# Kernel optimization log

Measured on AMD Instinct MI355X. Metric: run time of the kernel, lower is better.

The kernel has to match this reference:

```python
import jax, jax.numpy as jnp
import numpy as np

NEG_SLOPE = 0.2

def gat_conv(x, src, dst, W, a_s, a_d, b, num_nodes, heads, out_c, concat):
    # x: [N, F_in]; W: [F_in, heads*out_c]; a_s/a_d: [heads, out_c]
    h = (x @ W).reshape(num_nodes, heads, out_c)          # [N,H,C]
    alpha_src = jnp.sum(h * a_s, axis=-1)                 # [N,H]
    alpha_dst = jnp.sum(h * a_d, axis=-1)                 # [N,H]
    e = jax.nn.leaky_relu(alpha_src[src] + alpha_dst[dst], NEG_SLOPE)  # [E,H]
    m = jax.ops.segment_max(e, dst, num_segments=num_nodes)           # [N,H]
    e = jnp.exp(e - m[dst])
    s = jax.ops.segment_sum(e, dst, num_segments=num_nodes)
    alpha = e / (s[dst] + 1e-16)                          # [E,H]
    out = jax.ops.segment_sum(h[src] * alpha[:, :, None], dst, num_segments=num_nodes)  # [N,H,C]
    if concat:
        out = out.reshape(num_nodes, heads * out_c)
    else:
        out = out.mean(axis=1)
    return out + b


def setup_inputs() -> dict:
    key = jax.random.key(0)
    ks = jax.random.split(key, 16)
    N, E, P = 50000, 800000, 200000
    F_in, Hd, C_out, H = 128, 32, 64, 4
    inp = {
        'x': jax.random.normal(ks[0], (N, F_in), dtype=jnp.float32),
        'edge_index': jax.random.randint(ks[1], (2, E), 0, N, dtype=jnp.int32),
        'edge_pairs': jax.random.randint(ks[2], (2, P), 0, N, dtype=jnp.int32),
        'W1': jax.random.normal(ks[3], (F_in, H * Hd), dtype=jnp.float32) * 0.05,
        'att_src1': jax.random.normal(ks[4], (H, Hd), dtype=jnp.float32) * 0.05,
        'att_dst1': jax.random.normal(ks[5], (H, Hd), dtype=jnp.float32) * 0.05,
        'b1': jnp.zeros((H * Hd,), dtype=jnp.float32),
        'W2': jax.random.normal(ks[6], (H * Hd, C_out), dtype=jnp.float32) * 0.05,
        'att_src2': jax.random.normal(ks[7], (1, C_out), dtype=jnp.float32) * 0.05,
        'att_dst2': jax.random.normal(ks[8], (1, C_out), dtype=jnp.float32) * 0.05,
        'b2': jnp.zeros((C_out,), dtype=jnp.float32),
        'Wm1': jax.random.normal(ks[9], (2 * C_out, Hd), dtype=jnp.float32) * 0.05,
        'bm1': jnp.zeros((Hd,), dtype=jnp.float32),
        'Wm2': jax.random.normal(ks[10], (Hd, 1), dtype=jnp.float32) * 0.05,
        'bm2': jnp.zeros((1,), dtype=jnp.float32),
    }
    return inp


def reference(x, edge_index, edge_pairs, W1, att_src1, att_dst1, b1,
              W2, att_src2, att_dst2, b2, Wm1, bm1, Wm2, bm2):
    N = x.shape[0]
    # add self-loops (PyG GATConv default)
    loop = jnp.arange(N, dtype=edge_index.dtype)
    src = jnp.concatenate([edge_index[0], loop])
    dst = jnp.concatenate([edge_index[1], loop])
    h = gat_conv(x, src, dst, W1, att_src1, att_dst1, b1, N, 4, 32, concat=True)
    h = jax.nn.elu(h)
    h = gat_conv(h, src, dst, W2, att_src2, att_dst2, b2, N, 1, 64, concat=True)
    ps, pd = edge_pairs[0], edge_pairs[1]
    ef = jnp.concatenate([h[ps], h[pd]], axis=-1)          # [P, 2*C_out]
    out = jax.nn.relu(ef @ Wm1 + bm1) @ Wm2 + bm2          # [P,1]
    return out[:, 0]
```

## Files before the change

kernel.cpp:

```cpp
#include <hip/hip_runtime.h>
#include <hip/hip_bf16.h>
#include <hip/hip_fp16.h>


#define LRELU_SLOPE 0.2f
#define BKT_SH 7
#define NB_MAX 512

typedef _Float16 v8h __attribute__((ext_vector_type(8)));
typedef float    v4f __attribute__((ext_vector_type(4)));

__global__ void __launch_bounds__(256) zero_prep_kernel(
    const float* __restrict__ W1, const float* __restrict__ W2,
    const float* __restrict__ Wm1,
    _Float16* __restrict__ W1Th, _Float16* __restrict__ W2Th,
    float* __restrict__ Wm1T, uint4* __restrict__ zp, int zn4)
{
    int i = blockIdx.x * 256 + threadIdx.x;
    if (i < zn4) zp[i] = make_uint4(0u, 0u, 0u, 0u);
    if (i < 16384) {
        int k = i >> 7, j = i & 127;
        W1Th[j * 128 + k] = (_Float16)W1[i];
    } else if (i < 16384 + 8192) {
        int t = i - 16384;
        int k = t >> 6, j = t & 63;
        W2Th[j * 128 + k] = (_Float16)W2[t];
    } else if (i < 16384 + 8192 + 4096) {
        int t = i - 24576;
        int k = t >> 5, j = t & 31;
        Wm1T[j * 128 + k] = Wm1[t];
    }
}

template<int AHALF>
__device__ __forceinline__ void gemm_att_body(
    int bx, int by,
    const void* __restrict__ Xv, const _Float16* __restrict__ WTH,
    const float* __restrict__ atts, const float* __restrict__ attd,
    _Float16* __restrict__ OUT, float* __restrict__ oas, float* __restrict__ oad,
    int N, int ncols, int H, int headShift)
{
    __shared__ _Float16 cs[64 * 68];
    int tid = threadIdx.x;
    int lane = tid & 63;
    int wv = tid >> 6;
    int rowBase = bx * 64 + wv * 16;
    int colBase = by * 64;
    int lr = lane & 15;
    int lk = lane >> 4;

    v8h bf[4][4];
    #pragma unroll
    for (int ct = 0; ct < 4; ct++) {
        const _Float16* bp = WTH + (size_t)(colBase + ct * 16 + lr) * 128 + lk * 8;
        #pragma unroll
        for (int ks = 0; ks < 4; ks++)
            bf[ct][ks] = *(const v8h*)(bp + ks * 32);
    }

    int arow = rowBase + lr;
    if (arow >= N) arow = N - 1;
    v4f acc[4];
    #pragma unroll
    for (int ct = 0; ct < 4; ct++) acc[ct] = (v4f){0.f, 0.f, 0.f, 0.f};

    if (AHALF) {
        const _Float16* ap = (const _Float16*)Xv + (size_t)arow * 128 + lk * 8;
        #pragma unroll
        for (int ks = 0; ks < 4; ks++) {
            v8h af = *(const v8h*)(ap + ks * 32);
            #pragma unroll
            for (int ct = 0; ct < 4; ct++)
                acc[ct] = __builtin_amdgcn_mfma_f32_16x16x32_f16(af, bf[ct][ks],
                                                                 acc[ct], 0, 0, 0);
        }
    } else {
        const float* ap = (const float*)Xv + (size_t)arow * 128 + lk * 8;
        #pragma unroll
        for (int ks = 0; ks < 4; ks++) {
            float4 a0 = *(const float4*)(ap + ks * 32);
            float4 a1 = *(const float4*)(ap + ks * 32 + 4);
            v8h af;
            af[0] = (_Float16)a0.x; af[1] = (_Float16)a0.y;
            af[2] = (_Float16)a0.z; af[3] = (_Float16)a0.w;
            af[4] = (_Float16)a1.x; af[5] = (_Float16)a1.y;
            af[6] = (_Float16)a1.z; af[7] = (_Float16)a1.w;
            #pragma unroll
            for (int ct = 0; ct < 4; ct++)
                acc[ct] = __builtin_amdgcn_mfma_f32_16x16x32_f16(af, bf[ct][ks],
                                                                 acc[ct], 0, 0, 0);
        }
    }

    int ctPerHead = (1 << headShift) >> 4;
    #pragma unroll
    for (int hh = 0; hh < 2; hh++) {
        if (hh * ctPerHead >= 4) break;
        float ps[4] = {0.f, 0.f, 0.f, 0.f};
        float pd[4] = {0.f, 0.f, 0.f, 0.f};
        for (int c2 = 0; c2 < ctPerHead; c2++) {
            int ct = hh * ctPerHead + c2;
            int col = colBase + ct * 16 + lr;
            float ws = atts[col], wd = attd[col];
            #pragma unroll
            for (int r = 0; r < 4; r++) {
                ps[r] = fmaf(acc[ct][r], ws, ps[r]);
                pd[r] = fmaf(acc[ct][r], wd, pd[r]);
            }
        }
        #pragma unroll
        for (int r = 0; r < 4; r++) {
            #pragma unroll
            for (int m = 1; m < 16; m <<= 1) {
                ps[r] += __shfl_xor(ps[r], m);
                pd[r] += __shfl_xor(pd[r], m);
            }
        }
        if (lr == 0) {
            int head = (colBase >> headShift) + hh;
            #pragma unroll
            for (int r = 0; r < 4; r++) {
                int row = rowBase + lk * 4 + r;
                if (row < N) {
                    oas[(size_t)row * H + head] = ps[r];
                    oad[(size_t)row * H + head] = pd[r];
                }
            }
        }
    }

    #pragma unroll
    for (int ct = 0; ct < 4; ct++)
        #pragma unroll
        for (int r = 0; r < 4; r++)
            cs[(wv * 16 + lk * 4 + r) * 68 + ct * 16 + lr] = (_Float16)acc[ct][r];
    __syncthreads();
    int rr = tid >> 2;
    int cb = (tid & 3) * 16;
    int grow = bx * 64 + rr;
    if (grow < N) {
        const uint4* sp = (const uint4*)(cs + rr * 68 + cb);
        _Float16* op = OUT + (size_t)grow * ncols + colBase + cb;
        uint4 w0 = sp[0];
        uint4 w1 = sp[1];
        *(uint4*)op = w0;
        *(uint4*)(op + 8) = w1;
    }
}

__global__ void __launch_bounds__(256) gemm1_hist_kernel(
    const float* __restrict__ X, const _Float16* __restrict__ WTH,
    const float* __restrict__ atts, const float* __restrict__ attd,
    _Float16* __restrict__ OUT, float* __restrict__ oas, float* __restrict__ oad,
    int N, int nbG,
    const int* __restrict__ dst, int E, int* __restrict__ deg)
{
    if ((int)blockIdx.x < 2 * nbG) {
        gemm_att_body<0>(blockIdx.x % nbG, blockIdx.x / nbG, X, WTH, atts, attd,
                         OUT, oas, oad, N, 128, 4, 5);
    } else {
        int i = ((int)blockIdx.x - 2 * nbG) * 256 + threadIdx.x;
        if (i < E + N) {
            int d = (i < E) ? dst[i] : (i - E);
            atomicAdd(deg + d, 1);
        }
    }
}

__global__ void __launch_bounds__(256) gemm2_kernel(
    const _Float16* __restrict__ X, const _Float16* __restrict__ WTH,
    const float* __restrict__ atts, const float* __restrict__ attd,
    _Float16* __restrict__ OUT, float* __restrict__ oas, float* __restrict__ oad,
    int N)
{
    gemm_att_body<1>(blockIdx.x, 0, X, WTH, atts, attd, OUT, oas, oad,
                     N, 64, 1, 6);
}

__global__ void __launch_bounds__(1024) scan1_kernel(
    const int* __restrict__ deg, int* __restrict__ rowp,
    int* __restrict__ btot, int n)
{
    __shared__ int wsum[16];
    int t = threadIdx.x, lane = t & 63, wid = t >> 6;
    int idx = blockIdx.x * 1024 + t;
    int v = (idx < n) ? deg[idx] : 0;
    #pragma unroll
    for (int off = 1; off < 64; off <<= 1) {
        int y = __shfl_up(v, off);
        if (lane >= off) v += y;
    }
    if (lane == 63) wsum[wid] = v;
    __syncthreads();
    if (wid == 0) {
        int s = (lane < 16) ? wsum[lane] : 0;
        #pragma unroll
        for (int off = 1; off < 16; off <<= 1) {
            int y = __shfl_up(s, off);
            if (lane >= off) s += y;
        }
        if (lane < 16) wsum[lane] = s;
    }
    __syncthreads();
    if (wid > 0) v += wsum[wid - 1];
    if (idx < n) rowp[idx + 1] = v;
    if (t == 1023) btot[blockIdx.x] = v;
    if (idx == 0) rowp[0] = 0;
}

__global__ void __launch_bounds__(1024) scan23_kernel(
    int* __restrict__ rowp, const int* __restrict__ btot, int n)
{
    int b = blockIdx.x;
    if (b == 0) return;
    __shared__ int soff;
    int t = threadIdx.x;
    if (t < 64) {
        int v = (t < b) ? btot[t] : 0;
        #pragma unroll
        for (int m = 1; m < 64; m <<= 1) v += __shfl_xor(v, m);
        if (t == 0) soff = v;
    }
    __syncthreads();
    int idx = b * 1024 + t;
    if (idx < n) rowp[idx + 1] += soff;
}

__global__ void __launch_bounds__(256) bin_kernel(
    const int* __restrict__ src, const int* __restrict__ dst, int E, int N,
    const int* __restrict__ rowp, int* __restrict__ bcur,
    uint2* __restrict__ ebuf, int nbkt)
{
    __shared__ int lcnt[NB_MAX];
    __shared__ int loff[NB_MAX];
    __shared__ int lbase[NB_MAX];
    int tid = threadIdx.x;
    int EN = E + N;
    int base = blockIdx.x * 4096;
    for (int b = tid; b < nbkt; b += 256) { lcnt[b] = 0; loff[b] = 0; }
    __syncthreads();
    #pragma unroll
    for (int j = 0; j < 16; j++) {
        int i = base + j * 256 + tid;
        if (i < EN) {
            int d = (i < E) ? dst[i] : (i - E);
            atomicAdd(&lcnt[d >> BKT_SH], 1);
        }
    }
    __syncthreads();
    for (int b = tid; b < nbkt; b += 256) {
        int c = lcnt[b];
        lbase[b] = c ? atomicAdd(&bcur[b], c) : 0;
    }
    __syncthreads();
    #pragma unroll
    for (int j = 0; j < 16; j++) {
        int i = base + j * 256 + tid;
        if (i < EN) {
            int s, d;
            if (i < E) { s = src[i]; d = dst[i]; } else { s = d = i - E; }
            int b = d >> BKT_SH;
            int off = atomicAdd(&loff[b], 1);
            int nb0 = b << BKT_SH;
            int start = rowp[nb0 > N ? N : nb0];
            ebuf[(size_t)start + lbase[b] + off] = make_uint2((unsigned)d, (unsigned)s);
        }
    }
}

__global__ void __launch_bounds__(256) scatter2_kernel(
    const uint2* __restrict__ ebuf, const int* __restrict__ rowp,
    int* __restrict__ csrs, int N)
{
    __shared__ int lcur[1 << BKT_SH];
    int b = blockIdx.x;
    int n0 = b << BKT_SH;
    int n1 = n0 + (1 << BKT_SH); if (n1 > N) n1 = N;
    if (n0 >= N) return;
    for (int i = threadIdx.x; i < (1 << BKT_SH); i += 256) lcur[i] = 0;
    __syncthreads();
    int r0 = rowp[n0], r1 = rowp[n1];
    for (int i = r0 + threadIdx.x; i < r1; i += 256) {
        uint2 e = ebuf[i];
        int d = (int)e.x;
        int pos = rowp[d] + atomicAdd(&lcur[d - n0], 1);
        csrs[pos] = (int)e.y;
    }
}

template<int K>
__device__ __forceinline__ void chunk1(
    const int* __restrict__ csr, int base, int cnt,
    const float* __restrict__ as1, float adv,
    int el, int hh, int hd, int lane, const __half2* __restrict__ h1,
    float& accx, float& accy, float& srun)
{
    float wvA = 0.f, wvB = 0.f;
    if (el < cnt) {
        int s = csr[base + el];
        float e = as1[s * 4 + hh] + adv;
        e = e > 0.f ? e : LRELU_SLOPE * e;
        wvA = __expf(e);
    }
    if (K > 16 && el + 16 < cnt) {
        int s = csr[base + 16 + el];
        float e = as1[s * 4 + hh] + adv;
        e = e > 0.f ? e : LRELU_SLOPE * e;
        wvB = __expf(e);
    }
    float t = wvA + wvB;
    t += __shfl_xor(t, 4);  t += __shfl_xor(t, 8);
    t += __shfl_xor(t, 16); t += __shfl_xor(t, 32);
    srun += t;
    __half2 hv[K];
    #pragma unroll
    for (int e2 = 0; e2 < K; ++e2) {
        int ee = e2 < cnt ? e2 : cnt - 1;
        int s = csr[base + ee];
        hv[e2] = h1[(size_t)s * 64 + lane];
    }
    #pragma unroll
    for (int e2 = 0; e2 < K; ++e2) {
        float av = (e2 < 16) ? __shfl(wvA, (e2 << 2) | hd)
                             : __shfl(wvB, ((e2 - 16) << 2) | hd);
        float2 v = __half22float2(hv[e2]);
        accx = fmaf(av, v.x, accx);
        accy = fmaf(av, v.y, accy);
    }
}

__global__ void __launch_bounds__(256) edge1_kernel(
    const int* __restrict__ csr, const int* __restrict__ rowp,
    const __half2* __restrict__ h1, const float* __restrict__ as1,
    const float* __restrict__ ad1, const float* __restrict__ b1,
    __half* __restrict__ x2h, int N)
{
    int lane = threadIdx.x & 63;
    int n = __builtin_amdgcn_readfirstlane(blockIdx.x * 4 + (threadIdx.x >> 6));
    if (n >= N) return;
    int rs = rowp[n], re = rowp[n + 1];
    int hd = lane >> 4;
    int el = lane >> 2, hh = lane & 3;
    float adv = ad1[n * 4 + hh];
    float accx = 0.f, accy = 0.f, srun = 0.f;
    int base = rs, rem = re - rs;
    while (rem >= 32) {
        chunk1<32>(csr, base, 32, as1, adv, el, hh, hd, lane, h1, accx, accy, srun);
        base += 32; rem -= 32;
    }
    if (rem > 24)      chunk1<32>(csr, base, rem, as1, adv, el, hh, hd, lane, h1, accx, accy, srun);
    else if (rem > 16) chunk1<24>(csr, base, rem, as1, adv, el, hh, hd, lane, h1, accx, accy, srun);
    else if (rem > 8)  chunk1<16>(csr, base, rem, as1, adv, el, hh, hd, lane, h1, accx, accy, srun);
    else if (rem > 0)  chunk1<8> (csr, base, rem, as1, adv, el, hh, hd, lane, h1, accx, accy, srun);

    float sden = __shfl(srun, hd) + 1e-16f;
    float inv = 1.f / sden;
    float2 bv = *(const float2*)(b1 + lane * 2);
    float o0 = accx * inv + bv.x;
    float o1 = accy * inv + bv.y;
    o0 = o0 > 0.f ? o0 : (__expf(o0) - 1.f);
    o1 = o1 > 0.f ? o1 : (__expf(o1) - 1.f);
    *(__half2*)(x2h + (size_t)n * 128 + lane * 2) = __floats2half2_rn(o0, o1);
}

template<int K>
__device__ __forceinline__ void chunk2(
    const int* __restrict__ csr, int base, int cnt,
    const float* __restrict__ as2, float adv, int lane,
    const __half* __restrict__ h2, float& acc, float& srun)
{
    float wv = 0.f;
    if (lane < cnt) {
        int s = csr[base + lane];
        float e = as2[s] + adv;
        e = e > 0.f ? e : LRELU_SLOPE * e;
        wv = __expf(e);
    }
    srun += wv;
    __half hv[K];
    #pragma unroll
    for (int e2 = 0; e2 < K; ++e2) {
        int ee = e2 < cnt ? e2 : cnt - 1;
        int s = csr[base + ee];
        hv[e2] = h2[(size_t)s * 64 + lane];
    }
    #pragma unroll
    for (int e2 = 0; e2 < K; ++e2) {
        float av = __shfl(wv, e2);
        acc = fmaf(av, __half2float(hv[e2]), acc);
    }
}

__global__ void __launch_bounds__(256) edge2_kernel(
    const int* __restrict__ csr, const int* __restrict__ rowp,
    const __half* __restrict__ h2, const float* __restrict__ as2,
    const float* __restrict__ ad2, const float* __restrict__ b2,
    float* __restrict__ hf, int N)
{
    int lane = threadIdx.x & 63;
    int n = __builtin_amdgcn_readfirstlane(blockIdx.x * 4 + (threadIdx.x >> 6));
    if (n >= N) return;
    int rs = rowp[n], re = rowp[n + 1];
    float adv = ad2[n];
    float acc = 0.f, srun = 0.f;
    int base = rs, rem = re - rs;
    while (rem >= 16) {
        chunk2<16>(csr, base, 16, as2, adv, lane, h2, acc, srun);
        base += 16; rem -= 16;
    }
    if (rem > 8)      chunk2<16>(csr, base, rem, as2, adv, lane, h2, acc, srun);
    else if (rem > 0) chunk2<8> (csr, base, rem, as2, adv, lane, h2, acc, srun);

    #pragma unroll
    for (int m = 1; m < 64; m <<= 1) srun += __shfl_xor(srun, m);
    float o = acc / (srun + 1e-16f) + b2[lane];
    hf[(size_t)n * 64 + lane] = o;
}

__global__ void __launch_bounds__(256) node_mlp_kernel(
    const float* __restrict__ hf, const float* __restrict__ Wm1T,
    __half* __restrict__ uv, int N)
{
    int lane = threadIdx.x & 63;
    int j = lane & 31, half = lane >> 5;
    const float* wr = Wm1T + j * 128 + half * 64;
    float wreg[64];
    #pragma unroll
    for (int q = 0; q < 16; q++) {
        float4 t = ((const float4*)wr)[q];
        wreg[q*4] = t.x; wreg[q*4+1] = t.y; wreg[q*4+2] = t.z; wreg[q*4+3] = t.w;
    }
    int wgid = __builtin_amdgcn_readfirstlane(blockIdx.x * 4 + (threadIdx.x >> 6));
    int nwaves = gridDim.x * 4;
    for (int n = wgid; n < N; n += nwaves) {
        const float* hr = hf + (size_t)n * 64;
        float acc = 0.f;
        #pragma unroll
        for (int k = 0; k < 64; k += 4) {
            float4 hv = *(const float4*)(hr + k);
            acc = fmaf(hv.x, wreg[k],   acc);
            acc = fmaf(hv.y, wreg[k+1], acc);
            acc = fmaf(hv.z, wreg[k+2], acc);
            acc = fmaf(hv.w, wreg[k+3], acc);
        }
        uv[(size_t)n * 64 + lane] = __float2half_rn(acc);
    }
}

__global__ void __launch_bounds__(256) pair_mlp_kernel(
    const int* __restrict__ ps, const int* __restrict__ pd,
    const __half2* __restrict__ uv, const float* __restrict__ bm1,
    const float* __restrict__ Wm2, const float* __restrict__ bm2,
    float* __restrict__ out, int P)
{
    int gid = blockIdx.x * 256 + threadIdx.x;
    int p = gid >> 1;
    if (p >= P) return;
    int half = gid & 1;
    int j0 = half * 8;
    int a = ps[p], b = pd[p];
    const __half2* ua = uv + (size_t)a * 32 + j0;
    const __half2* vb = uv + (size_t)b * 32 + 16 + j0;
    float r = 0.f;
    #pragma unroll
    for (int q = 0; q < 8; q++) {
        float2 uu = __half22float2(ua[q]);
        float2 vv = __half22float2(vb[q]);
        float2 bb = *(const float2*)(bm1 + half * 16 + q * 2);
        float2 ww = *(const float2*)(Wm2 + half * 16 + q * 2);
        float h0 = uu.x + vv.x + bb.x; h0 = h0 > 0.f ? h0 : 0.f; r = fmaf(h0, ww.x, r);
        float h1 = uu.y + vv.y + bb.y; h1 = h1 > 0.f ? h1 : 0.f; r = fmaf(h1, ww.y, r);
    }
    r += __shfl_xor(r, 1);
    if (half == 0) out[p] = r + bm2[0];
}

extern "C" void kernel_launch(void* const* d_in, const int* in_sizes, int n_in,
                              void* d_out, int out_size, void* d_ws, size_t ws_size,
                              hipStream_t stream)
{
    const float* x    = (const float*)d_in[0];
    const int*   ei   = (const int*)  d_in[1];
    const int*   ep   = (const int*)  d_in[2];
    const float* W1   = (const float*)d_in[3];
    const float* atS1 = (const float*)d_in[4];
    const float* atD1 = (const float*)d_in[5];
    const float* b1   = (const float*)d_in[6];
    const float* W2   = (const float*)d_in[7];
    const float* atS2 = (const float*)d_in[8];
    const float* atD2 = (const float*)d_in[9];
    const float* b2   = (const float*)d_in[10];
    const float* Wm1  = (const float*)d_in[11];
    const float* bm1  = (const float*)d_in[12];
    const float* Wm2  = (const float*)d_in[13];
    const float* bm2  = (const float*)d_in[14];
    float* out = (float*)d_out;

    int N = in_sizes[0] / 128;
    int E = in_sizes[1] / 2;
    int P = in_sizes[2] / 2;
    int Etot = E + N;

    char* w = (char*)d_ws;
    auto alloc = [&](size_t bytes) {
        char* p = w; w += (bytes + 255) & ~(size_t)255; return p;
    };
    _Float16* W1Th = (_Float16*)alloc(16384 * 2);
    _Float16* W2Th = (_Float16*)alloc(8192 * 2);
    float*    Wm1T = (float*)alloc(4096 * 4);
    _Float16* h1   = (_Float16*)alloc((size_t)N * 128 * 2);
    __half*   x2h  = (__half*)alloc((size_t)N * 128 * 2);
    _Float16* h2   = (_Float16*)alloc((size_t)N * 64 * 2);
    float*    hf   = (float*)alloc((size_t)N * 64 * 4);
    int*      rowp = (int*)alloc((size_t)(N + 1) * 4);
    int*      btot = (int*)alloc(64 * 4);
    int*      csrs = (int*)alloc((size_t)Etot * 4);
    uint2*    ebuf = (uint2*)alloc((size_t)Etot * 8);
    char* z0 = w;
    int*   deg  = (int*)alloc((size_t)N * 4);
    int*   bcur = (int*)alloc(NB_MAX * 4);
    char* z1 = w;
    float* as1  = (float*)alloc((size_t)N * 4 * 4);
    float* ad1  = (float*)alloc((size_t)N * 4 * 4);
    float* as2  = (float*)alloc((size_t)N * 4);
    float* ad2  = (float*)alloc((size_t)N * 4);
    __half* uv = (__half*)alloc((size_t)N * 64 * 2);

    int zn4 = (int)((z1 - z0) / 16);
    zero_prep_kernel<<<112, 256, 0, stream>>>(W1, W2, Wm1, W1Th, W2Th, Wm1T,
                                              (uint4*)z0, zn4);

    int EN = E + N;
    int nbG = (N + 63) / 64;
    int nbH = (EN + 255) / 256;
    gemm1_hist_kernel<<<2 * nbG + nbH, 256, 0, stream>>>(
        x, W1Th, atS1, atD1, h1, as1, ad1, N, nbG, ei + E, E, deg);

    int nb = (N + 1023) / 1024;
    scan1_kernel<<<nb, 1024, 0, stream>>>(deg, rowp, btot, N);
    scan23_kernel<<<nb, 1024, 0, stream>>>(rowp, btot, N);
    int nbkt = (N + (1 << BKT_SH) - 1) >> BKT_SH;
    bin_kernel<<<(EN + 4095) / 4096, 256, 0, stream>>>(ei, ei + E, E, N, rowp,
                                                       bcur, ebuf, nbkt);
    scatter2_kernel<<<nbkt, 256, 0, stream>>>(ebuf, rowp, csrs, N);

    edge1_kernel<<<(N + 3) / 4, 256, 0, stream>>>(csrs, rowp, (const __half2*)h1,
                                                  as1, ad1, b1, x2h, N);
    gemm2_kernel<<<nbG, 256, 0, stream>>>((const _Float16*)x2h, W2Th, atS2, atD2,
                                          h2, as2, ad2, N);
    edge2_kernel<<<(N + 3) / 4, 256, 0, stream>>>(csrs, rowp, (const __half*)h2,
                                                  as2, ad2, b2, hf, N);

    node_mlp_kernel<<<1024, 256, 0, stream>>>(hf, Wm1T, uv, N);
    pair_mlp_kernel<<<(2 * P + 255) / 256, 256, 0, stream>>>(ep, ep + P,
                                                             (const __half2*)uv,
                                                             bm1, Wm2, bm2, out, P);
}
```

Measured before the change: 204.6 us.

## Replace per-node degree histogram with bucket-level counting in CSR construction

The CSR build no longer runs a global per-node degree histogram followed by a two-kernel scan over all nodes. The GEMM1 kernel now runs a per-block bucket count whose per-block bases go to a workspace array. A single-block scan then covers the ~391 buckets, a second pass bins the edges using the stored bases, and a build kernel computes per-node degrees and row pointers inside each bucket in shared memory. This removes one kernel launch and the global atomics on 50k degree counters, at the cost of reading the edge list twice and adding an extra workspace buffer.

```diff
diff --git a/kernel.cpp b/kernel.cpp
--- a/kernel.cpp
+++ b/kernel.cpp
@@ -148,22 +148,44 @@
     }
 }
 
-__global__ void __launch_bounds__(256) gemm1_hist_kernel(
+__device__ __forceinline__ void passA_body(
+    int blk, const int* __restrict__ src, const int* __restrict__ dst,
+    int E, int N, int* __restrict__ bktcnt, int* __restrict__ lbase_g, int nbkt)
+{
+    __shared__ int lcnt[NB_MAX];
+    int tid = threadIdx.x;
+    int EN = E + N;
+    int base = blk * 4096;
+    for (int b = tid; b < nbkt; b += 256) lcnt[b] = 0;
+    __syncthreads();
+    #pragma unroll
+    for (int j = 0; j < 16; j++) {
+        int i = base + j * 256 + tid;
+        if (i < EN) {
+            int d = (i < E) ? dst[i] : (i - E);
+            atomicAdd(&lcnt[d >> BKT_SH], 1);
+        }
+    }
+    __syncthreads();
+    for (int b = tid; b < nbkt; b += 256) {
+        int c = lcnt[b];
+        lbase_g[(size_t)blk * nbkt + b] = c ? atomicAdd(&bktcnt[b], c) : 0;
+    }
+}
+
+__global__ void __launch_bounds__(256) gemm1_passA_kernel(
     const float* __restrict__ X, const _Float16* __restrict__ WTH,
     const float* __restrict__ atts, const float* __restrict__ attd,
     _Float16* __restrict__ OUT, float* __restrict__ oas, float* __restrict__ oad,
     int N, int nbG,
-    const int* __restrict__ dst, int E, int* __restrict__ deg)
+    const int* __restrict__ src, const int* __restrict__ dst, int E,
+    int* __restrict__ bktcnt, int* __restrict__ lbase_g, int nbkt)
 {
     if ((int)blockIdx.x < 2 * nbG) {
         gemm_att_body<0>(blockIdx.x % nbG, blockIdx.x / nbG, X, WTH, atts, attd,
                          OUT, oas, oad, N, 128, 4, 5);
     } else {
-        int i = ((int)blockIdx.x - 2 * nbG) * 256 + threadIdx.x;
-        if (i < E + N) {
-            int d = (i < E) ? dst[i] : (i - E);
-            atomicAdd(deg + d, 1);
-        }
+        passA_body((int)blockIdx.x - 2 * nbG, src, dst, E, N, bktcnt, lbase_g, nbkt);
     }
 }
 
@@ -177,14 +199,12 @@
                      N, 64, 1, 6);
 }
 
-__global__ void __launch_bounds__(1024) scan1_kernel(
-    const int* __restrict__ deg, int* __restrict__ rowp,
-    int* __restrict__ btot, int n)
-{
-    __shared__ int wsum[16];
+__global__ void __launch_bounds__(512) scanb_kernel(
+    const int* __restrict__ bktcnt, int* __restrict__ bktoff, int nbkt)
+{
+    __shared__ int wsum[8];
     int t = threadIdx.x, lane = t & 63, wid = t >> 6;
-    int idx = blockIdx.x * 1024 + t;
-    int v = (idx < n) ? deg[idx] : 0;
+    int v = (t < nbkt) ? bktcnt[t] : 0;
     #pragma unroll
     for (int off = 1; off < 64; off <<= 1) {
         int y = __shfl_up(v, off);
@@ -193,64 +213,34 @@
     if (lane == 63) wsum[wid] = v;
     __syncthreads();
     if (wid == 0) {
-        int s = (lane < 16) ? wsum[lane] : 0;
-        #pragma unroll
-        for (int off = 1; off < 16; off <<= 1) {
+        int s = (lane < 8) ? wsum[lane] : 0;
+        #pragma unroll
+        for (int off = 1; off < 8; off <<= 1) {
             int y = __shfl_up(s, off);
             if (lane >= off) s += y;
         }
-        if (lane < 16) wsum[lane] = s;
+        if (lane < 8) wsum[lane] = s;
     }
     __syncthreads();
     if (wid > 0) v += wsum[wid - 1];
-    if (idx < n) rowp[idx + 1] = v;
-    if (t == 1023) btot[blockIdx.x] = v;
-    if (idx == 0) rowp[0] = 0;
-}
-
-__global__ void __launch_bounds__(1024) scan23_kernel(
-    int* __restrict__ rowp, const int* __restrict__ btot, int n)
-{
-    int b = blockIdx.x;
-    if (b == 0) return;
-    __shared__ int soff;
-    int t = threadIdx.x;
-    if (t < 64) {
-        int v = (t < b) ? btot[t] : 0;
-        #pragma unroll
-        for (int m = 1; m < 64; m <<= 1) v += __shfl_xor(v, m);
-        if (t == 0) soff = v;
-    }
-    __syncthreads();
-    int idx = b * 1024 + t;
-    if (idx < n) rowp[idx + 1] += soff;
-}
-
-__global__ void __launch_bounds__(256) bin_kernel(
+    if (t < nbkt) bktoff[t + 1] = v;
+    if (t == 0) bktoff[0] = 0;
+}
+
+__global__ void __launch_bounds__(256) passB_kernel(
     const int* __restrict__ src, const int* __restrict__ dst, int E, int N,
-    const int* __restrict__ rowp, int* __restrict__ bcur,
+    const int* __restrict__ bktoff, const int* __restrict__ lbase_g,
     uint2* __restrict__ ebuf, int nbkt)
 {
-    __shared__ int lcnt[NB_MAX];
+    __shared__ int sbase[NB_MAX];
     __shared__ int loff[NB_MAX];
-    __shared__ int lbase[NB_MAX];
+    int blk = blockIdx.x;
     int tid = threadIdx.x;
     int EN = E + N;
-    int base = blockIdx.x * 4096;
-    for (int b = tid; b < nbkt; b += 256) { lcnt[b] = 0; loff[b] = 0; }
-    __syncthreads();
-    #pragma unroll
-    for (int j = 0; j < 16; j++) {
-        int i = base + j * 256 + tid;
-        if (i < EN) {
-            int d = (i < E) ? dst[i] : (i - E);
-            atomicAdd(&lcnt[d >> BKT_SH], 1);
-        }
-    }
-    __syncthreads();
+    int base = blk * 4096;
     for (int b = tid; b < nbkt; b += 256) {
-        int c = lcnt[b];
-        lbase[b] = c ? atomicAdd(&bcur[b], c) : 0;
+        sbase[b] = bktoff[b] + lbase_g[(size_t)blk * nbkt + b];
+        loff[b] = 0;
     }
     __syncthreads();
     #pragma unroll
@@ -261,29 +251,48 @@
             if (i < E) { s = src[i]; d = dst[i]; } else { s = d = i - E; }
             int b = d >> BKT_SH;
             int off = atomicAdd(&loff[b], 1);
-            int nb0 = b << BKT_SH;
-            int start = rowp[nb0 > N ? N : nb0];
-            ebuf[(size_t)start + lbase[b] + off] = make_uint2((unsigned)d, (unsigned)s);
-        }
-    }
-}
-
-__global__ void __launch_bounds__(256) scatter2_kernel(
-    const uint2* __restrict__ ebuf, const int* __restrict__ rowp,
-    int* __restrict__ csrs, int N)
-{
-    __shared__ int lcur[1 << BKT_SH];
+            ebuf[(size_t)sbase[b] + off] = make_uint2((unsigned)d, (unsigned)s);
+        }
+    }
+}
+
+__global__ void __launch_bounds__(256) build_kernel(
+    const uint2* __restrict__ ebuf, const int* __restrict__ bktoff,
+    int* __restrict__ rowp, int* __restrict__ csrs, int N, int nbkt)
+{
+    __shared__ int ldeg[128];
+    __shared__ int lrow[129];
+    __shared__ int lcur[128];
+    __shared__ int w0tot;
     int b = blockIdx.x;
+    if (b >= nbkt) return;
     int n0 = b << BKT_SH;
-    int n1 = n0 + (1 << BKT_SH); if (n1 > N) n1 = N;
-    if (n0 >= N) return;
-    for (int i = threadIdx.x; i < (1 << BKT_SH); i += 256) lcur[i] = 0;
-    __syncthreads();
-    int r0 = rowp[n0], r1 = rowp[n1];
-    for (int i = r0 + threadIdx.x; i < r1; i += 256) {
+    int n1 = n0 + 128; if (n1 > N) n1 = N;
+    int r0 = bktoff[b], r1 = bktoff[b + 1];
+    int t = threadIdx.x;
+    if (t < 128) { ldeg[t] = 0; lcur[t] = 0; }
+    __syncthreads();
+    for (int i = r0 + t; i < r1; i += 256)
+        atomicAdd(&ldeg[(int)ebuf[i].x - n0], 1);
+    __syncthreads();
+    int lane = t & 63;
+    int v = (t < 128) ? ldeg[t] : 0;
+    #pragma unroll
+    for (int off = 1; off < 64; off <<= 1) {
+        int y = __shfl_up(v, off);
+        if (lane >= off) v += y;
+    }
+    if (t == 63) w0tot = v;
+    __syncthreads();
+    if (t >= 64 && t < 128) v += w0tot;
+    if (t < 128) lrow[t + 1] = v;
+    if (t == 0) { lrow[0] = 0; rowp[n0] = r0; }
+    if (t < n1 - n0) rowp[n0 + t + 1] = r0 + v;
+    __syncthreads();
+    for (int i = r0 + t; i < r1; i += 256) {
         uint2 e = ebuf[i];
-        int d = (int)e.x;
-        int pos = rowp[d] + atomicAdd(&lcur[d - n0], 1);
+        int d = (int)e.x - n0;
+        int pos = r0 + lrow[d] + atomicAdd(&lcur[d], 1);
         csrs[pos] = (int)e.y;
     }
 }
@@ -500,6 +509,9 @@
     int E = in_sizes[1] / 2;
     int P = in_sizes[2] / 2;
     int Etot = E + N;
+    int EN = Etot;
+    int nbkt = (N + (1 << BKT_SH) - 1) >> BKT_SH;
+    int nbA  = (EN + 4095) / 4096;
 
     char* w = (char*)d_ws;
     auto alloc = [&](size_t bytes) {
@@ -513,12 +525,12 @@
     _Float16* h2   = (_Float16*)alloc((size_t)N * 64 * 2);
     float*    hf   = (float*)alloc((size_t)N * 64 * 4);
     int*      rowp = (int*)alloc((size_t)(N + 1) * 4);
-    int*      btot = (int*)alloc(64 * 4);
+    int*      bktoff = (int*)alloc((size_t)(nbkt + 1) * 4);
     int*      csrs = (int*)alloc((size_t)Etot * 4);
     uint2*    ebuf = (uint2*)alloc((size_t)Etot * 8);
+    int*      lbase_g = (int*)alloc((size_t)nbA * nbkt * 4);
     char* z0 = w;
-    int*   deg  = (int*)alloc((size_t)N * 4);
-    int*   bcur = (int*)alloc(NB_MAX * 4);
+    int*   bktcnt = (int*)alloc(NB_MAX * 4);
     char* z1 = w;
     float* as1  = (float*)alloc((size_t)N * 4 * 4);
     float* ad1  = (float*)alloc((size_t)N * 4 * 4);
@@ -530,19 +542,15 @@
     zero_prep_kernel<<<112, 256, 0, stream>>>(W1, W2, Wm1, W1Th, W2Th, Wm1T,
                                               (uint4*)z0, zn4);
 
-    int EN = E + N;
     int nbG = (N + 63) / 64;
-    int nbH = (EN + 255) / 256;
-    gemm1_hist_kernel<<<2 * nbG + nbH, 256, 0, stream>>>(
-        x, W1Th, atS1, atD1, h1, as1, ad1, N, nbG, ei + E, E, deg);
-
-    int nb = (N + 1023) / 1024;
-    scan1_kernel<<<nb, 1024, 0, stream>>>(deg, rowp, btot, N);
-    scan23_kernel<<<nb, 1024, 0, stream>>>(rowp, btot, N);
-    int nbkt = (N + (1 << BKT_SH) - 1) >> BKT_SH;
-    bin_kernel<<<(EN + 4095) / 4096, 256, 0, stream>>>(ei, ei + E, E, N, rowp,
-                                                       bcur, ebuf, nbkt);
-    scatter2_kernel<<<nbkt, 256, 0, stream>>>(ebuf, rowp, csrs, N);
+    gemm1_passA_kernel<<<2 * nbG + nbA, 256, 0, stream>>>(
+        x, W1Th, atS1, atD1, h1, as1, ad1, N, nbG,
+        ei, ei + E, E, bktcnt, lbase_g, nbkt);
+
+    scanb_kernel<<<1, 512, 0, stream>>>(bktcnt, bktoff, nbkt);
+    passB_kernel<<<nbA, 256, 0, stream>>>(ei, ei + E, E, N, bktoff, lbase_g,
+                                          ebuf, nbkt);
+    build_kernel<<<nbkt, 256, 0, stream>>>(ebuf, bktoff, rowp, csrs, N, nbkt);
 
     edge1_kernel<<<(N + 3) / 4, 256, 0, stream>>>(csrs, rowp, (const __half2*)h1,
                                                   as1, ad1, b1, x2h, N);
```

Result: faster. 169.3 us (median of 3 runs) (-17.3%).
